# Performance work log

Hardware: AMD Instinct MI355X
Metric: run time of the kernel (lower is better)

The kernel has to match this reference:

```python
import jax, jax.numpy as jnp
import numpy as np

B, S, DMODEL = 1, 2048, 4096
H, HKV, DH = 32, 8, 128
LTAB, RBKT = 20, 128
NEG = -1e9


def rotate_half(x):
    x1, x2 = x[..., : x.shape[-1] // 2], x[..., x.shape[-1] // 2:]
    return jnp.concatenate((-x2, x1), axis=-1)


def setup_inputs() -> dict:
    key = jax.random.key(0)
    ks = jax.random.split(key, 12)
    inp = {
        "hidden_states": jax.random.normal(ks[0], (B, S, DMODEL), jnp.float32),
        "cos": jax.random.uniform(ks[1], (B, S, DH), jnp.float32),
        "sin": jax.random.uniform(ks[2], (B, S, DH), jnp.float32),
        "q_probs": jax.random.uniform(ks[3], (B, H, LTAB, RBKT), jnp.float32),
        "v_norm": jax.random.uniform(ks[4], (B, H, S), jnp.float32),
        "allowed": jnp.ones((B, H, S), dtype=bool),
        "k_hard": jax.random.randint(ks[5], (B, H, LTAB, S), 0, RBKT, jnp.int32),
        "Wq": jax.random.normal(ks[6], (DMODEL, H * DH), jnp.float32) * 0.02,
        "Wk": jax.random.normal(ks[7], (DMODEL, HKV * DH), jnp.float32) * 0.02,
        "Wv": jax.random.normal(ks[8], (DMODEL, HKV * DH), jnp.float32) * 0.02,
        "Wo": jax.random.normal(ks[9], (H * DH, DMODEL), jnp.float32) * 0.02,
        "sink": 4,
        "window": 128,
        "M": 256,
    }
    return inp


def _sparse_key_mask(q_probs, v_norm, allowed, k_hard, sink, window, M):
    """Faithful jax version of build_sparse_list_decode, returned as a boolean
    allowed-key mask [B, H, T] (equivalent to scattering sparse_list)."""
    Bm, Hm, _, T = k_hard.shape
    # soft-hash collision score: sum over tables of q bucket prob at key's bucket,
    # weighted by value-norm history, restricted to allowed keys.
    coll = jnp.take_along_axis(q_probs, k_hard.astype(jnp.int32), axis=-1).sum(axis=2)  # [B,H,T]
    scores = jnp.where(allowed, coll * v_norm, -jnp.inf)
    M_eff = min(M, T)
    mask = jnp.zeros((Bm, Hm, T), dtype=bool)
    if M_eff > 0:
        heavy_idx = jax.lax.top_k(scores, M_eff)[1]  # [B,H,M]
        b_ix = jnp.arange(Bm)[:, None, None]
        h_ix = jnp.arange(Hm)[None, :, None]
        mask = mask.at[b_ix, h_ix, heavy_idx].set(True)
    sink = max(0, min(sink, T))
    window = max(0, min(window, T))
    if sink > 0:
        mask = mask.at[:, :, :sink].set(True)
    if window > 0:
        win_start = max(T - window, sink)
        if win_start < T:
            mask = mask.at[:, :, win_start:].set(True)
    if sink == 0 and window == 0:
        mask = mask.at[:, :, T - 1].set(True)
    return mask & allowed


def reference(hidden_states, cos, sin, q_probs, v_norm, allowed, k_hard,
              Wq, Wk, Wv, Wo, sink, window, M):
    Bx, Sx, _ = hidden_states.shape
    scaling = DH ** -0.5
    q = (hidden_states @ Wq).reshape(Bx, Sx, H, DH).transpose(0, 2, 1, 3)   # [B,H,S,Dh]
    k = (hidden_states @ Wk).reshape(Bx, Sx, HKV, DH).transpose(0, 2, 1, 3)  # [B,Hkv,S,Dh]
    v = (hidden_states @ Wv).reshape(Bx, Sx, HKV, DH).transpose(0, 2, 1, 3)
    # RoPE (unsqueeze_dim=1)
    c, s = cos[:, None, :, :], sin[:, None, :, :]
    q = q * c + rotate_half(q) * s
    k = k * c + rotate_half(k) * s
    # repeat_kv for GQA
    n_rep = H // HKV
    k = jnp.repeat(k, n_rep, axis=1)
    v = jnp.repeat(v, n_rep, axis=1)
    # sparse heavy-hitter + sink + window key mask (no_grad in the original)
    key_mask = _sparse_key_mask(q_probs, v_norm, allowed, k_hard, sink, window, M)  # [B,H,S]
    causal = jnp.tril(jnp.ones((Sx, Sx), dtype=bool))
    allow = causal[None, None] & key_mask[:, :, None, :]  # [B,H,S,S]
    scores = jnp.einsum('bhqd,bhkd->bhqk', q, k) * scaling
    attn = jax.nn.softmax(jnp.where(allow, scores, NEG), axis=-1)
    out = jnp.einsum('bhqk,bhkd->bhqd', attn, v)
    out = out.transpose(0, 2, 1, 3).reshape(Bx, Sx, H * DH)
    return out @ Wo
```

## Files before the change

### kernel.cpp

```cpp
#include <hip/hip_runtime.h>
#include <hip/hip_bf16.h>
#include <cstdint>
#include <cstddef>

namespace {

constexpr int S_LEN = 2048;
constexpr int DM    = 4096;
constexpr int NH    = 32;
constexpr int NKV   = 8;
constexpr int DH    = 128;
constexpr int LTAB  = 20;
constexpr int RBKT  = 128;
constexpr int NQKV  = NH * DH + 2 * NKV * DH;
constexpr int KOFF  = NH * DH;
constexpr int VOFF  = NH * DH + NKV * DH;

typedef short s16x8 __attribute__((ext_vector_type(8)));
typedef float f32x4 __attribute__((ext_vector_type(4)));
typedef unsigned long long u64;
struct u64x2 { u64 x, y; };

__device__ inline short bf16s(float f) {
  __hip_bfloat16 b = __float2bfloat16(f);
  return (short)*reinterpret_cast<unsigned short*>(&b);
}
__device__ inline float s2f(short s) {
  unsigned short u = (unsigned short)s;
  return __bfloat162float(*reinterpret_cast<__hip_bfloat16*>(&u));
}

__device__ inline void transpose64_body(const float* __restrict__ W,
                                        __hip_bfloat16* __restrict__ Wt, int N, int bx,
                                        int by, int tid, float (*tile)[65]) {
  const int kb = by * 64, nb = bx * 64;
  const int r0 = tid >> 4, c4 = (tid & 15) * 4;
#pragma unroll
  for (int it = 0; it < 4; ++it) {
    const int r = r0 + it * 16;
    float4 v = *reinterpret_cast<const float4*>(&W[(size_t)(kb + r) * N + nb + c4]);
    tile[r][c4] = v.x;
    tile[r][c4 + 1] = v.y;
    tile[r][c4 + 2] = v.z;
    tile[r][c4 + 3] = v.w;
  }
  __syncthreads();
  const int n0 = tid >> 4, k4 = (tid & 15) * 4;
#pragma unroll
  for (int it = 0; it < 4; ++it) {
    const int n = n0 + it * 16;
    ushort4 o;
    o.x = (unsigned short)bf16s(tile[k4][n]);
    o.y = (unsigned short)bf16s(tile[k4 + 1][n]);
    o.z = (unsigned short)bf16s(tile[k4 + 2][n]);
    o.w = (unsigned short)bf16s(tile[k4 + 3][n]);
    *reinterpret_cast<ushort4*>(&Wt[(size_t)(nb + n) * DM + kb + k4]) = o;
  }
}

__global__ __launch_bounds__(256) void prep_kernel(
    const float* __restrict__ hidden, const float* __restrict__ Wq,
    const float* __restrict__ Wk, const float* __restrict__ Wv,
    const float* __restrict__ Wo, __hip_bfloat16* __restrict__ hbf,
    __hip_bfloat16* __restrict__ WqkvT, __hip_bfloat16* __restrict__ WoT) {
  __shared__ float tile[64][65];
  const int b = blockIdx.x, tid = threadIdx.x;
  if (b < 2048) {
    const size_t base = (size_t)b * 1024;
#pragma unroll
    for (int it = 0; it < 4; ++it) {
      const size_t i = base + it * 256 + tid;
      float4 v = reinterpret_cast<const float4*>(hidden)[i];
      ushort4 o;
      o.x = (unsigned short)bf16s(v.x);
      o.y = (unsigned short)bf16s(v.y);
      o.z = (unsigned short)bf16s(v.z);
      o.w = (unsigned short)bf16s(v.w);
      reinterpret_cast<ushort4*>(hbf)[i] = o;
    }
    return;
  }
  const float* W;
  __hip_bfloat16* Wt;
  int N, bx, by;
  int t = b - 2048;
  if (t < 4096) {
    W = Wq; Wt = WqkvT; N = DM; bx = t & 63; by = t >> 6;
  } else if (t < 5120) {
    t -= 4096; W = Wk; Wt = WqkvT + (size_t)KOFF * DM; N = NKV * DH; bx = t & 15; by = t >> 4;
  } else if (t < 6144) {
    t -= 5120; W = Wv; Wt = WqkvT + (size_t)VOFF * DM; N = NKV * DH; bx = t & 15; by = t >> 4;
  } else {
    t -= 6144; W = Wo; Wt = WoT; N = DM; bx = t & 63; by = t >> 6;
  }
  transpose64_body(W, Wt, N, bx, by, tid, tile);
}

__global__ __launch_bounds__(1024) void select_kernel(const float* __restrict__ q_probs,
                                                      const float* __restrict__ v_norm,
                                                      const int* __restrict__ allowed,
                                                      const int* __restrict__ k_hard,
                                                      const int* __restrict__ sinkp,
                                                      const int* __restrict__ winp,
                                                      const int* __restrict__ Mp,
                                                      int* __restrict__ sel_idx,
                                                      int* __restrict__ sel_cnt) {
  const int h = blockIdx.x;
  const int tid = threadIdx.x;
  const int lane = tid & 63;
  const int wid = tid >> 6;
  __shared__ u64 keys[S_LEN];
  __shared__ int waveTot[16];
  const int t0 = tid * 2;
  float c0 = 0.f, c1 = 0.f;
#pragma unroll
  for (int l = 0; l < LTAB; ++l) {
    const int2 kh = *reinterpret_cast<const int2*>(&k_hard[(size_t)(h * LTAB + l) * S_LEN + t0]);
    c0 += q_probs[(h * LTAB + l) * RBKT + kh.x];
    c1 += q_probs[(h * LTAB + l) * RBKT + kh.y];
  }
  const int2 al = *reinterpret_cast<const int2*>(&allowed[h * S_LEN + t0]);
  const float2 vn = *reinterpret_cast<const float2*>(&v_norm[h * S_LEN + t0]);
  const float s0 = al.x ? c0 * vn.x : -INFINITY;
  const float s1 = al.y ? c1 * vn.y : -INFINITY;
  auto mkkey = [](float s, int t) -> u64 {
    unsigned m = __float_as_uint(s);
    m = (m & 0x80000000u) ? ~m : (m | 0x80000000u);
    return ((u64)m << 11) | (u64)(S_LEN - 1 - t);
  };
  const u64 k0 = mkkey(s0, t0);
  const u64 k1 = mkkey(s1, t0 + 1);
  keys[t0] = k0;
  keys[t0 + 1] = k1;
  __syncthreads();
  int r0 = 0, r1 = 0;
#pragma unroll 8
  for (int u = 0; u < S_LEN; u += 2) {
    const u64x2 kv = *reinterpret_cast<const u64x2*>(&keys[u]);
    r0 += (kv.x > k0) + (kv.y > k0);
    r1 += (kv.x > k1) + (kv.y > k1);
  }
  const int Mv = min(Mp[0], S_LEN);
  int sv = sinkp[0];
  sv = sv < 0 ? 0 : (sv > S_LEN ? S_LEN : sv);
  int wv = winp[0];
  wv = wv < 0 ? 0 : (wv > S_LEN ? S_LEN : wv);
  int wstart = S_LEN - wv;
  if (wstart < sv) wstart = sv;
  bool sel0 = r0 < Mv, sel1 = r1 < Mv;
  if (t0 < sv) sel0 = true;
  if (t0 + 1 < sv) sel1 = true;
  if (wv > 0) {
    if (t0 >= wstart) sel0 = true;
    if (t0 + 1 >= wstart) sel1 = true;
  }
  if (sv == 0 && wv == 0) {
    if (t0 == S_LEN - 1) sel0 = true;
    if (t0 + 1 == S_LEN - 1) sel1 = true;
  }
  sel0 = sel0 && (al.x != 0);
  sel1 = sel1 && (al.y != 0);
  const int cnt = (sel0 ? 1 : 0) + (sel1 ? 1 : 0);
  int inc = cnt;
#pragma unroll
  for (int off = 1; off < 64; off <<= 1) {
    int n = __shfl_up(inc, off);
    if (lane >= off) inc += n;
  }
  if (lane == 63) waveTot[wid] = inc;
  __syncthreads();
  int wbase = 0;
  for (int w = 0; w < wid; ++w) wbase += waveTot[w];
  int pos = wbase + inc - cnt;
  if (tid == 0) {
    int tot = 0;
#pragma unroll
    for (int w = 0; w < 16; ++w) tot += waveTot[w];
    sel_cnt[h] = tot;
  }
  if (sel0) sel_idx[h * S_LEN + pos++] = t0;
  if (sel1) sel_idx[h * S_LEN + pos] = t0 + 1;
}

template <bool OUT_F32>
__global__ __launch_bounds__(256) void gemm_bt(const __hip_bfloat16* __restrict__ A,
                                               const __hip_bfloat16* __restrict__ Bt,
                                               void* __restrict__ Cout,
                                               int N, int K) {
  __shared__ __hip_bfloat16 As[128 * 64];
  __shared__ __hip_bfloat16 Bs[128 * 64];
  const int tid = threadIdx.x;
  const int wid = tid >> 6;
  const int lane = tid & 63;
  const int bm = blockIdx.y, bn = blockIdx.x;
  const int wr = wid >> 1, wc = wid & 1;
  f32x4 acc[4][4] = {};
  const __hip_bfloat16* Abase = A + (size_t)bm * 128 * K;
  const __hip_bfloat16* Bbase = Bt + (size_t)bn * 128 * K;
  for (int kt = 0; kt < K; kt += 64) {
    __syncthreads();
#pragma unroll
    for (int j = 0; j < 4; ++j) {
      const int pb = j * 4096 + wid * 1024;
      const int p = pb + lane * 16;
      const int row = p >> 7;
      const int slot = ((p >> 4) & 7) ^ (row & 7);
      const int goff = row * K + kt + slot * 8;
      __builtin_amdgcn_global_load_lds(
          (const __attribute__((address_space(1))) void*)(Abase + goff),
          (__attribute__((address_space(3))) void*)(As + (pb >> 1)), 16, 0, 0);
      __builtin_amdgcn_global_load_lds(
          (const __attribute__((address_space(1))) void*)(Bbase + goff),
          (__attribute__((address_space(3))) void*)(Bs + (pb >> 1)), 16, 0, 0);
    }
    __syncthreads();
#pragma unroll
    for (int kk = 0; kk < 2; ++kk) {
      s16x8 af[4], bf[4];
#pragma unroll
      for (int i = 0; i < 4; ++i) {
        const int ra = wr * 64 + i * 16 + (lane & 15);
        const int sa = (kk * 4 + (lane >> 4)) ^ (ra & 7);
        af[i] = *reinterpret_cast<const s16x8*>(As + ra * 64 + sa * 8);
        const int rb = wc * 64 + i * 16 + (lane & 15);
        const int sb = (kk * 4 + (lane >> 4)) ^ (rb & 7);
        bf[i] = *reinterpret_cast<const s16x8*>(Bs + rb * 64 + sb * 8);
      }
#pragma unroll
      for (int i = 0; i < 4; ++i)
#pragma unroll
        for (int jn = 0; jn < 4; ++jn)
          acc[i][jn] = __builtin_amdgcn_mfma_f32_16x16x32_bf16(af[i], bf[jn], acc[i][jn], 0, 0, 0);
    }
  }
  const int rg = (lane >> 4) * 4;
  const int cg = lane & 15;
#pragma unroll
  for (int i = 0; i < 4; ++i)
#pragma unroll
    for (int jn = 0; jn < 4; ++jn)
#pragma unroll
      for (int r = 0; r < 4; ++r) {
        const int rr = bm * 128 + wr * 64 + i * 16 + rg + r;
        const int cc = bn * 128 + wc * 64 + jn * 16 + cg;
        if (OUT_F32)
          reinterpret_cast<float*>(Cout)[(size_t)rr * N + cc] = acc[i][jn][r];
        else
          reinterpret_cast<__hip_bfloat16*>(Cout)[(size_t)rr * N + cc] =
              __float2bfloat16(acc[i][jn][r]);
      }
}

__global__ __launch_bounds__(256) void gemm_bt_splitk(const __hip_bfloat16* __restrict__ A,
                                                      const __hip_bfloat16* __restrict__ Bt,
                                                      float* __restrict__ P,
                                                      int N, int Kfull, int KH) {
  __shared__ __hip_bfloat16 As[128 * 64];
  __shared__ __hip_bfloat16 Bs[128 * 64];
  const int tid = threadIdx.x;
  const int wid = tid >> 6;
  const int lane = tid & 63;
  const int bm = blockIdx.y, bn = blockIdx.x, kz = blockIdx.z;
  const int wr = wid >> 1, wc = wid & 1;
  f32x4 acc[4][4] = {};
  const __hip_bfloat16* Abase = A + (size_t)bm * 128 * Kfull + kz * KH;
  const __hip_bfloat16* Bbase = Bt + (size_t)bn * 128 * Kfull + kz * KH;
  for (int kt = 0; kt < KH; kt += 64) {
    __syncthreads();
#pragma unroll
    for (int j = 0; j < 4; ++j) {
      const int pb = j * 4096 + wid * 1024;
      const int p = pb + lane * 16;
      const int row = p >> 7;
      const int slot = ((p >> 4) & 7) ^ (row & 7);
      const int goff = row * Kfull + kt + slot * 8;
      __builtin_amdgcn_global_load_lds(
          (const __attribute__((address_space(1))) void*)(Abase + goff),
          (__attribute__((address_space(3))) void*)(As + (pb >> 1)), 16, 0, 0);
      __builtin_amdgcn_global_load_lds(
          (const __attribute__((address_space(1))) void*)(Bbase + goff),
          (__attribute__((address_space(3))) void*)(Bs + (pb >> 1)), 16, 0, 0);
    }
    __syncthreads();
#pragma unroll
    for (int kk = 0; kk < 2; ++kk) {
      s16x8 af[4], bf[4];
#pragma unroll
      for (int i = 0; i < 4; ++i) {
        const int ra = wr * 64 + i * 16 + (lane & 15);
        const int sa = (kk * 4 + (lane >> 4)) ^ (ra & 7);
        af[i] = *reinterpret_cast<const s16x8*>(As + ra * 64 + sa * 8);
        const int rb = wc * 64 + i * 16 + (lane & 15);
        const int sb = (kk * 4 + (lane >> 4)) ^ (rb & 7);
        bf[i] = *reinterpret_cast<const s16x8*>(Bs + rb * 64 + sb * 8);
      }
#pragma unroll
      for (int i = 0; i < 4; ++i)
#pragma unroll
        for (int jn = 0; jn < 4; ++jn)
          acc[i][jn] = __builtin_amdgcn_mfma_f32_16x16x32_bf16(af[i], bf[jn], acc[i][jn], 0, 0, 0);
    }
  }
  float* Pz = P + (size_t)kz * S_LEN * N;
  const int rg = (lane >> 4) * 4;
  const int cg = lane & 15;
#pragma unroll
  for (int i = 0; i < 4; ++i)
#pragma unroll
    for (int jn = 0; jn < 4; ++jn)
#pragma unroll
      for (int r = 0; r < 4; ++r) {
        const int rr = bm * 128 + wr * 64 + i * 16 + rg + r;
        const int cc = bn * 128 + wc * 64 + jn * 16 + cg;
        Pz[(size_t)rr * N + cc] = acc[i][jn][r];
      }
}

__global__ __launch_bounds__(256) void reduce_splitk(const float* __restrict__ P,
                                                     float* __restrict__ out, int n4) {
  const int i = blockIdx.x * 256 + threadIdx.x;
  if (i >= n4) return;
  const float4 a = reinterpret_cast<const float4*>(P)[i];
  const float4 b = reinterpret_cast<const float4*>(P + (size_t)S_LEN * DM)[i];
  float4 o;
  o.x = a.x + b.x;
  o.y = a.y + b.y;
  o.z = a.z + b.z;
  o.w = a.w + b.w;
  reinterpret_cast<float4*>(out)[i] = o;
}

__global__ __launch_bounds__(256) void rope_kernel(const __hip_bfloat16* __restrict__ QKV,
                                                   const float* __restrict__ cosb,
                                                   const float* __restrict__ sinb,
                                                   __hip_bfloat16* __restrict__ Qro,
                                                   __hip_bfloat16* __restrict__ Kro) {
  const int s = blockIdx.x;
  const int tid = threadIdx.x;
  const float* cs = cosb + s * DH;
  const float* sn = sinb + s * DH;
  const __hip_bfloat16* row = QKV + (size_t)s * NQKV;
  for (int ch = tid; ch < 512 + 128; ch += 256) {
    const bool isQ = ch < 512;
    const int idx8 = (isQ ? ch : ch - 512) * 8;
    const int d8 = idx8 & (DH - 1);
    const int hb = idx8 - d8;
    const __hip_bfloat16* src = isQ ? row : row + KOFF;
    s16x8 v = *reinterpret_cast<const s16x8*>(src + idx8);
    s16x8 p = *reinterpret_cast<const s16x8*>(src + hb + (d8 ^ 64));
    const float sgn = (d8 < 64) ? -1.f : 1.f;
    s16x8 outv;
#pragma unroll
    for (int j = 0; j < 8; ++j) {
      const float r = s2f(v[j]) * cs[d8 + j] + sgn * s2f(p[j]) * sn[d8 + j];
      outv[j] = bf16s(r);
    }
    if (isQ)
      *reinterpret_cast<s16x8*>(Qro + (size_t)s * (NH * DH) + idx8) = outv;
    else
      *reinterpret_cast<s16x8*>(Kro + (size_t)s * (NKV * DH) + idx8) = outv;
  }
}

__global__ __launch_bounds__(256) void attn_kernel(const __hip_bfloat16* __restrict__ Qro,
                                                   const __hip_bfloat16* __restrict__ Kro,
                                                   const __hip_bfloat16* __restrict__ Vpk,
                                                   const int* __restrict__ sel_idx,
                                                   const int* __restrict__ sel_cnt,
                                                   __hip_bfloat16* __restrict__ ctx) {
  constexpr int BKV = 64;
  const int h = blockIdx.y;
  const int q0 = blockIdx.x * 64;
  const int tid = threadIdx.x, wid = tid >> 6, lane = tid & 63;
  const int l15 = lane & 15, hi = lane >> 4;
  const int kv = h >> 2;
  __shared__ __hip_bfloat16 Ks[BKV][DH + 8];
  __shared__ __hip_bfloat16 Vt[DH][BKV + 8];
  __shared__ __hip_bfloat16 Ps[4][16][BKV + 8];
  __shared__ int tIdx[BKV];
  const int qbase = q0 + wid * 16;
  const float scaling = 0.08838834764831845f;
  s16x8 qf[4];
  {
    const __hip_bfloat16* qp =
        Qro + (size_t)(qbase + l15) * (NH * DH) + h * DH + hi * 8;
#pragma unroll
    for (int kt = 0; kt < 4; ++kt) {
      s16x8 q = *reinterpret_cast<const s16x8*>(qp + kt * 32);
#pragma unroll
      for (int j = 0; j < 8; ++j) q[j] = bf16s(s2f(q[j]) * scaling);
      qf[kt] = q;
    }
  }
  s16x8 ones;
#pragma unroll
  for (int j = 0; j < 8; ++j) ones[j] = (short)0x3F80;
  float mr[4], lr[4];
#pragma unroll
  for (int r = 0; r < 4; ++r) {
    mr[r] = -3.0e38f;
    lr[r] = 0.f;
  }
  f32x4 o[8] = {};
  const int cnt = sel_cnt[h];
  const int qmax = q0 + 63;
  for (int j0 = 0; j0 < cnt; j0 += BKV) {
    if (sel_idx[h * S_LEN + j0] > qmax) break;
    const int nk = min(BKV, cnt - j0);
    __syncthreads();
    if (tid < BKV) tIdx[tid] = (tid < nk) ? sel_idx[h * S_LEN + j0 + tid] : 0x7fffffff;
#pragma unroll
    for (int c = 0; c < 4; ++c) {
      const int ch = tid + c * 256;
      const int row = ch >> 4, c8 = ch & 15;
      if (row < nk) {
        const int t = sel_idx[h * S_LEN + j0 + row];
        *reinterpret_cast<s16x8*>(&Ks[row][c8 * 8]) = *reinterpret_cast<const s16x8*>(
            Kro + (size_t)t * (NKV * DH) + kv * DH + c8 * 8);
      }
    }
    {
      const int j = tid >> 2;
      const int dp = (tid & 3) * 32;
      const int ccA = j ^ (((dp >> 4) & 7) << 3);
      const int ccB = j ^ ((((dp >> 4) + 1) & 7) << 3);
      if (j < nk) {
        const int t = sel_idx[h * S_LEN + j0 + j];
        const __hip_bfloat16* vp = Vpk + (size_t)t * NQKV + kv * DH + dp;
        s16x8 a = *reinterpret_cast<const s16x8*>(vp);
        s16x8 bq = *reinterpret_cast<const s16x8*>(vp + 8);
        s16x8 cq = *reinterpret_cast<const s16x8*>(vp + 16);
        s16x8 dq = *reinterpret_cast<const s16x8*>(vp + 24);
#pragma unroll
        for (int i = 0; i < 8; ++i) reinterpret_cast<short&>(Vt[dp + i][ccA]) = a[i];
#pragma unroll
        for (int i = 0; i < 8; ++i) reinterpret_cast<short&>(Vt[dp + 8 + i][ccA]) = bq[i];
#pragma unroll
        for (int i = 0; i < 8; ++i) reinterpret_cast<short&>(Vt[dp + 16 + i][ccB]) = cq[i];
#pragma unroll
        for (int i = 0; i < 8; ++i) reinterpret_cast<short&>(Vt[dp + 24 + i][ccB]) = dq[i];
      } else {
#pragma unroll
        for (int i = 0; i < 16; ++i) reinterpret_cast<short&>(Vt[dp + i][ccA]) = 0;
#pragma unroll
        for (int i = 0; i < 16; ++i) reinterpret_cast<short&>(Vt[dp + 16 + i][ccB]) = 0;
      }
    }
    __syncthreads();
    f32x4 sc[4];
#pragma unroll
    for (int kc = 0; kc < 4; ++kc) sc[kc] = f32x4{0.f, 0.f, 0.f, 0.f};
#pragma unroll
    for (int kt = 0; kt < 4; ++kt) {
#pragma unroll
      for (int kc = 0; kc < 4; ++kc) {
        const s16x8 kf =
            *reinterpret_cast<const s16x8*>(&Ks[kc * 16 + l15][kt * 32 + hi * 8]);
        sc[kc] = __builtin_amdgcn_mfma_f32_16x16x32_bf16(qf[kt], kf, sc[kc], 0, 0, 0);
      }
    }
    int tt[4];
#pragma unroll
    for (int kc = 0; kc < 4; ++kc) tt[kc] = tIdx[kc * 16 + l15];
    float vv[4][4];
    bool need = false;
#pragma unroll
    for (int r = 0; r < 4; ++r) {
      const int qs = qbase + (hi << 2) + r;
      float mx = -3.0e38f;
#pragma unroll
      for (int kc = 0; kc < 4; ++kc) {
        vv[kc][r] = (tt[kc] <= qs) ? sc[kc][r] : -1.0e9f;
        mx = fmaxf(mx, vv[kc][r]);
      }
      need = need || (mx > mr[r] + 8.f);
    }
    if (__any(need)) {
#pragma unroll
      for (int r = 0; r < 4; ++r) {
        float m = fmaxf(fmaxf(vv[0][r], vv[1][r]), fmaxf(vv[2][r], vv[3][r]));
#pragma unroll
        for (int off = 1; off < 16; off <<= 1) m = fmaxf(m, __shfl_xor(m, off));
        const float mn = fmaxf(mr[r], m);
        const float scl = __expf(mr[r] - mn);
        lr[r] *= scl;
#pragma unroll
        for (int nt = 0; nt < 8; ++nt) o[nt][r] *= scl;
        mr[r] = mn;
      }
    }
#pragma unroll
    for (int r = 0; r < 4; ++r) {
#pragma unroll
      for (int kc = 0; kc < 4; ++kc) {
        Ps[wid][(hi << 2) + r][kc * 16 + l15] = __float2bfloat16(__expf(vv[kc][r] - mr[r]));
      }
    }
    const s16x8 pf0 = *reinterpret_cast<const s16x8*>(&Ps[wid][l15][hi * 8]);
    const s16x8 pf1 = *reinterpret_cast<const s16x8*>(&Ps[wid][l15][32 + hi * 8]);
    {
      f32x4 zero = {0.f, 0.f, 0.f, 0.f};
      f32x4 ps = __builtin_amdgcn_mfma_f32_16x16x32_bf16(pf0, ones, zero, 0, 0, 0);
      ps = __builtin_amdgcn_mfma_f32_16x16x32_bf16(pf1, ones, ps, 0, 0, 0);
#pragma unroll
      for (int r = 0; r < 4; ++r) lr[r] += ps[r];
    }
#pragma unroll
    for (int nt = 0; nt < 8; ++nt) {
      const s16x8 vfa =
          *reinterpret_cast<const s16x8*>(&Vt[nt * 16 + l15][(hi * 8) ^ (nt * 8)]);
      const s16x8 vfb =
          *reinterpret_cast<const s16x8*>(&Vt[nt * 16 + l15][(32 + hi * 8) ^ (nt * 8)]);
      o[nt] = __builtin_amdgcn_mfma_f32_16x16x32_bf16(pf0, vfa, o[nt], 0, 0, 0);
      o[nt] = __builtin_amdgcn_mfma_f32_16x16x32_bf16(pf1, vfb, o[nt], 0, 0, 0);
    }
  }
#pragma unroll
  for (int nt = 0; nt < 8; ++nt)
#pragma unroll
    for (int r = 0; r < 4; ++r) {
      const int qs = qbase + (hi << 2) + r;
      const int d = nt * 16 + l15;
      ctx[(size_t)qs * (NH * DH) + h * DH + d] = __float2bfloat16(o[nt][r] / lr[r]);
    }
}

}

extern "C" void kernel_launch(void* const* d_in, const int* in_sizes, int n_in,
                              void* d_out, int out_size, void* d_ws, size_t ws_size,
                              hipStream_t stream) {
  const float* hidden = (const float*)d_in[0];
  const float* cosb = (const float*)d_in[1];
  const float* sinb = (const float*)d_in[2];
  const float* q_probs = (const float*)d_in[3];
  const float* v_norm = (const float*)d_in[4];
  const int* allowed = (const int*)d_in[5];
  const int* k_hard = (const int*)d_in[6];
  const float* Wq = (const float*)d_in[7];
  const float* Wk = (const float*)d_in[8];
  const float* Wv = (const float*)d_in[9];
  const float* Wo = (const float*)d_in[10];
  const int* sinkp = (const int*)d_in[11];
  const int* winp = (const int*)d_in[12];
  const int* Mp = (const int*)d_in[13];

  char* ws = (char*)d_ws;
  size_t off = 0;
  auto alloc = [&](size_t bytes) -> char* {
    char* p = ws + off;
    off += (bytes + 255) & ~(size_t)255;
    return p;
  };
  __hip_bfloat16* hbf = (__hip_bfloat16*)alloc((size_t)S_LEN * DM * 2);
  __hip_bfloat16* WqkvT = (__hip_bfloat16*)alloc((size_t)NQKV * DM * 2);
  __hip_bfloat16* WoT = (__hip_bfloat16*)alloc((size_t)DM * DM * 2);
  __hip_bfloat16* QKV = (__hip_bfloat16*)alloc((size_t)S_LEN * NQKV * 2);
  __hip_bfloat16* Qro = (__hip_bfloat16*)alloc((size_t)S_LEN * NH * DH * 2);
  __hip_bfloat16* Kro = (__hip_bfloat16*)alloc((size_t)S_LEN * NKV * DH * 2);
  __hip_bfloat16* ctx = (__hip_bfloat16*)alloc((size_t)S_LEN * NH * DH * 2);
  int* sel_idx = (int*)alloc((size_t)NH * S_LEN * 4);
  int* sel_cnt = (int*)alloc((size_t)NH * 4);
  if (off > ws_size) return;
  float* Psplit = (float*)hbf;

  prep_kernel<<<12288, 256, 0, stream>>>(hidden, Wq, Wk, Wv, Wo, hbf, WqkvT, WoT);

  select_kernel<<<NH, 1024, 0, stream>>>(q_probs, v_norm, allowed, k_hard, sinkp, winp, Mp,
                                         sel_idx, sel_cnt);

  gemm_bt<false><<<dim3(NQKV / 128, S_LEN / 128), 256, 0, stream>>>(
      hbf, WqkvT, (void*)QKV, NQKV, DM);

  rope_kernel<<<S_LEN, 256, 0, stream>>>(QKV, cosb, sinb, Qro, Kro);

  attn_kernel<<<dim3(S_LEN / 64, NH), 256, 0, stream>>>(Qro, Kro, QKV + VOFF, sel_idx,
                                                        sel_cnt, ctx);

  gemm_bt_splitk<<<dim3(DM / 128, S_LEN / 128, 2), 256, 0, stream>>>(ctx, WoT, Psplit, DM,
                                                                     DM, DM / 2);
  reduce_splitk<<<(S_LEN * DM / 4 + 255) / 256, 256, 0, stream>>>((const float*)Psplit,
                                                                  (float*)d_out,
                                                                  S_LEN * DM / 4);
}
```

Before: 409.4 us.

## Fuse RoPE into QKV GEMM epilogue and prefetch attention K/V tiles into registers

The QKV projection GEMM now stages its output tile through shared memory and applies RoPE to Q and K columns in the epilogue, writing rotated values in place. This removes the separate rope kernel launch and its extra global read and write of Q and K. The attention kernel reads Q, K and V directly from the packed QKV buffer. It also double-buffers K/V gathers in registers, loading the next tile while the current one is computed, to hide gather latency. In exchange the GEMM epilogue gains two barriers and per-row cos/sin loads, and the attention kernel uses more registers.

```diff
diff --git a/kernel.cpp b/kernel.cpp
--- a/kernel.cpp
+++ b/kernel.cpp
@@ -182,13 +182,15 @@
   if (sel1) sel_idx[h * S_LEN + pos] = t0 + 1;
 }
 
-template <bool OUT_F32>
-__global__ __launch_bounds__(256) void gemm_bt(const __hip_bfloat16* __restrict__ A,
-                                               const __hip_bfloat16* __restrict__ Bt,
-                                               void* __restrict__ Cout,
-                                               int N, int K) {
-  __shared__ __hip_bfloat16 As[128 * 64];
-  __shared__ __hip_bfloat16 Bs[128 * 64];
+__global__ __launch_bounds__(256) void gemm_qkv_rope(const __hip_bfloat16* __restrict__ A,
+                                                     const __hip_bfloat16* __restrict__ Bt,
+                                                     __hip_bfloat16* __restrict__ Cout,
+                                                     const float* __restrict__ cosb,
+                                                     const float* __restrict__ sinb) {
+  __shared__ __hip_bfloat16 smbuf[128 * 136];
+  __hip_bfloat16* As = smbuf;
+  __hip_bfloat16* Bs = smbuf + 128 * 64;
+  constexpr int N = NQKV, K = DM;
   const int tid = threadIdx.x;
   const int wid = tid >> 6;
   const int lane = tid & 63;
@@ -233,6 +235,7 @@
           acc[i][jn] = __builtin_amdgcn_mfma_f32_16x16x32_bf16(af[i], bf[jn], acc[i][jn], 0, 0, 0);
     }
   }
+  __syncthreads();
   const int rg = (lane >> 4) * 4;
   const int cg = lane & 15;
 #pragma unroll
@@ -240,15 +243,32 @@
 #pragma unroll
     for (int jn = 0; jn < 4; ++jn)
 #pragma unroll
-      for (int r = 0; r < 4; ++r) {
-        const int rr = bm * 128 + wr * 64 + i * 16 + rg + r;
-        const int cc = bn * 128 + wc * 64 + jn * 16 + cg;
-        if (OUT_F32)
-          reinterpret_cast<float*>(Cout)[(size_t)rr * N + cc] = acc[i][jn][r];
-        else
-          reinterpret_cast<__hip_bfloat16*>(Cout)[(size_t)rr * N + cc] =
-              __float2bfloat16(acc[i][jn][r]);
-      }
+      for (int r = 0; r < 4; ++r)
+        smbuf[(wr * 64 + i * 16 + rg + r) * 136 + wc * 64 + jn * 16 + cg] =
+            __float2bfloat16(acc[i][jn][r]);
+  __syncthreads();
+  const bool isV = (bn * 128) >= VOFF;
+  const int srow = tid >> 1;
+  const int col0 = (tid & 1) * 64;
+  const int sg = bm * 128 + srow;
+#pragma unroll
+  for (int c = 0; c < 8; ++c) {
+    const int d0 = col0 + ((c + srow) & 7) * 8;
+    s16x8 x = *reinterpret_cast<const s16x8*>(&smbuf[srow * 136 + d0]);
+    s16x8 outv;
+    if (isV) {
+      outv = x;
+    } else {
+      const s16x8 xp = *reinterpret_cast<const s16x8*>(&smbuf[srow * 136 + (d0 ^ 64)]);
+      const float sgn = (d0 < 64) ? -1.f : 1.f;
+      const float* cs = cosb + (size_t)sg * DH + d0;
+      const float* sn = sinb + (size_t)sg * DH + d0;
+#pragma unroll
+      for (int j = 0; j < 8; ++j)
+        outv[j] = bf16s(s2f(x[j]) * cs[j] + sgn * s2f(xp[j]) * sn[j]);
+    }
+    *reinterpret_cast<s16x8*>(&Cout[(size_t)sg * N + bn * 128 + d0]) = outv;
+  }
 }
 
 __global__ __launch_bounds__(256) void gemm_bt_splitk(const __hip_bfloat16* __restrict__ A,
@@ -330,41 +350,7 @@
   reinterpret_cast<float4*>(out)[i] = o;
 }
 
-__global__ __launch_bounds__(256) void rope_kernel(const __hip_bfloat16* __restrict__ QKV,
-                                                   const float* __restrict__ cosb,
-                                                   const float* __restrict__ sinb,
-                                                   __hip_bfloat16* __restrict__ Qro,
-                                                   __hip_bfloat16* __restrict__ Kro) {
-  const int s = blockIdx.x;
-  const int tid = threadIdx.x;
-  const float* cs = cosb + s * DH;
-  const float* sn = sinb + s * DH;
-  const __hip_bfloat16* row = QKV + (size_t)s * NQKV;
-  for (int ch = tid; ch < 512 + 128; ch += 256) {
-    const bool isQ = ch < 512;
-    const int idx8 = (isQ ? ch : ch - 512) * 8;
-    const int d8 = idx8 & (DH - 1);
-    const int hb = idx8 - d8;
-    const __hip_bfloat16* src = isQ ? row : row + KOFF;
-    s16x8 v = *reinterpret_cast<const s16x8*>(src + idx8);
-    s16x8 p = *reinterpret_cast<const s16x8*>(src + hb + (d8 ^ 64));
-    const float sgn = (d8 < 64) ? -1.f : 1.f;
-    s16x8 outv;
-#pragma unroll
-    for (int j = 0; j < 8; ++j) {
-      const float r = s2f(v[j]) * cs[d8 + j] + sgn * s2f(p[j]) * sn[d8 + j];
-      outv[j] = bf16s(r);
-    }
-    if (isQ)
-      *reinterpret_cast<s16x8*>(Qro + (size_t)s * (NH * DH) + idx8) = outv;
-    else
-      *reinterpret_cast<s16x8*>(Kro + (size_t)s * (NKV * DH) + idx8) = outv;
-  }
-}
-
-__global__ __launch_bounds__(256) void attn_kernel(const __hip_bfloat16* __restrict__ Qro,
-                                                   const __hip_bfloat16* __restrict__ Kro,
-                                                   const __hip_bfloat16* __restrict__ Vpk,
+__global__ __launch_bounds__(256) void attn_kernel(const __hip_bfloat16* __restrict__ Qkv,
                                                    const int* __restrict__ sel_idx,
                                                    const int* __restrict__ sel_cnt,
                                                    __hip_bfloat16* __restrict__ ctx) {
@@ -383,7 +369,7 @@
   s16x8 qf[4];
   {
     const __hip_bfloat16* qp =
-        Qro + (size_t)(qbase + l15) * (NH * DH) + h * DH + hi * 8;
+        Qkv + (size_t)(qbase + l15) * NQKV + h * DH + hi * 8;
 #pragma unroll
     for (int kt = 0; kt < 4; ++kt) {
       s16x8 q = *reinterpret_cast<const s16x8*>(qp + kt * 32);
@@ -404,115 +390,129 @@
   f32x4 o[8] = {};
   const int cnt = sel_cnt[h];
   const int qmax = q0 + 63;
-  for (int j0 = 0; j0 < cnt; j0 += BKV) {
-    if (sel_idx[h * S_LEN + j0] > qmax) break;
+
+  int tIdxReg = 0x7fffffff;
+  s16x8 rK[4];
+  s16x8 rV[4];
+  const int vj = tid >> 2, vdp = (tid & 3) * 32;
+
+  auto load_tile = [&](int j0) {
     const int nk = min(BKV, cnt - j0);
-    __syncthreads();
-    if (tid < BKV) tIdx[tid] = (tid < nk) ? sel_idx[h * S_LEN + j0 + tid] : 0x7fffffff;
+    if (tid < BKV) tIdxReg = (tid < nk) ? sel_idx[h * S_LEN + j0 + tid] : 0x7fffffff;
 #pragma unroll
     for (int c = 0; c < 4; ++c) {
       const int ch = tid + c * 256;
       const int row = ch >> 4, c8 = ch & 15;
-      if (row < nk) {
-        const int t = sel_idx[h * S_LEN + j0 + row];
-        *reinterpret_cast<s16x8*>(&Ks[row][c8 * 8]) = *reinterpret_cast<const s16x8*>(
-            Kro + (size_t)t * (NKV * DH) + kv * DH + c8 * 8);
-      }
-    }
-    {
-      const int j = tid >> 2;
-      const int dp = (tid & 3) * 32;
-      const int ccA = j ^ (((dp >> 4) & 7) << 3);
-      const int ccB = j ^ ((((dp >> 4) + 1) & 7) << 3);
-      if (j < nk) {
-        const int t = sel_idx[h * S_LEN + j0 + j];
-        const __hip_bfloat16* vp = Vpk + (size_t)t * NQKV + kv * DH + dp;
-        s16x8 a = *reinterpret_cast<const s16x8*>(vp);
-        s16x8 bq = *reinterpret_cast<const s16x8*>(vp + 8);
-        s16x8 cq = *reinterpret_cast<const s16x8*>(vp + 16);
-        s16x8 dq = *reinterpret_cast<const s16x8*>(vp + 24);
-#pragma unroll
-        for (int i = 0; i < 8; ++i) reinterpret_cast<short&>(Vt[dp + i][ccA]) = a[i];
-#pragma unroll
-        for (int i = 0; i < 8; ++i) reinterpret_cast<short&>(Vt[dp + 8 + i][ccA]) = bq[i];
-#pragma unroll
-        for (int i = 0; i < 8; ++i) reinterpret_cast<short&>(Vt[dp + 16 + i][ccB]) = cq[i];
-#pragma unroll
-        for (int i = 0; i < 8; ++i) reinterpret_cast<short&>(Vt[dp + 24 + i][ccB]) = dq[i];
-      } else {
-#pragma unroll
-        for (int i = 0; i < 16; ++i) reinterpret_cast<short&>(Vt[dp + i][ccA]) = 0;
-#pragma unroll
-        for (int i = 0; i < 16; ++i) reinterpret_cast<short&>(Vt[dp + 16 + i][ccB]) = 0;
-      }
-    }
-    __syncthreads();
-    f32x4 sc[4];
-#pragma unroll
-    for (int kc = 0; kc < 4; ++kc) sc[kc] = f32x4{0.f, 0.f, 0.f, 0.f};
-#pragma unroll
-    for (int kt = 0; kt < 4; ++kt) {
-#pragma unroll
-      for (int kc = 0; kc < 4; ++kc) {
-        const s16x8 kf =
-            *reinterpret_cast<const s16x8*>(&Ks[kc * 16 + l15][kt * 32 + hi * 8]);
-        sc[kc] = __builtin_amdgcn_mfma_f32_16x16x32_bf16(qf[kt], kf, sc[kc], 0, 0, 0);
-      }
-    }
-    int tt[4];
-#pragma unroll
-    for (int kc = 0; kc < 4; ++kc) tt[kc] = tIdx[kc * 16 + l15];
-    float vv[4][4];
-    bool need = false;
-#pragma unroll
-    for (int r = 0; r < 4; ++r) {
-      const int qs = qbase + (hi << 2) + r;
-      float mx = -3.0e38f;
-#pragma unroll
-      for (int kc = 0; kc < 4; ++kc) {
-        vv[kc][r] = (tt[kc] <= qs) ? sc[kc][r] : -1.0e9f;
-        mx = fmaxf(mx, vv[kc][r]);
-      }
-      need = need || (mx > mr[r] + 8.f);
-    }
-    if (__any(need)) {
+      const int t = sel_idx[h * S_LEN + j0 + min(row, nk - 1)];
+      rK[c] = *reinterpret_cast<const s16x8*>(Qkv + (size_t)t * NQKV + KOFF + kv * DH + c8 * 8);
+    }
+    if (vj < nk) {
+      const int t = sel_idx[h * S_LEN + j0 + vj];
+      const __hip_bfloat16* vp = Qkv + (size_t)t * NQKV + VOFF + kv * DH + vdp;
+#pragma unroll
+      for (int c = 0; c < 4; ++c) rV[c] = *reinterpret_cast<const s16x8*>(vp + c * 8);
+    } else {
+#pragma unroll
+      for (int c = 0; c < 4; ++c) rV[c] = s16x8{};
+    }
+  };
+
+  if (cnt > 0 && sel_idx[h * S_LEN] <= qmax) {
+    load_tile(0);
+    for (int j0 = 0; j0 < cnt; j0 += BKV) {
+      const int nk = min(BKV, cnt - j0);
+      __syncthreads();
+      if (tid < BKV) tIdx[tid] = tIdxReg;
+#pragma unroll
+      for (int c = 0; c < 4; ++c) {
+        const int ch = tid + c * 256;
+        const int row = ch >> 4, c8 = ch & 15;
+        if (row < nk) *reinterpret_cast<s16x8*>(&Ks[row][c8 * 8]) = rK[c];
+      }
+      {
+        const int ccA = vj ^ (((vdp >> 4) & 7) << 3);
+        const int ccB = vj ^ ((((vdp >> 4) + 1) & 7) << 3);
+#pragma unroll
+        for (int i = 0; i < 8; ++i) reinterpret_cast<short&>(Vt[vdp + i][ccA]) = rV[0][i];
+#pragma unroll
+        for (int i = 0; i < 8; ++i) reinterpret_cast<short&>(Vt[vdp + 8 + i][ccA]) = rV[1][i];
+#pragma unroll
+        for (int i = 0; i < 8; ++i) reinterpret_cast<short&>(Vt[vdp + 16 + i][ccB]) = rV[2][i];
+#pragma unroll
+        for (int i = 0; i < 8; ++i) reinterpret_cast<short&>(Vt[vdp + 24 + i][ccB]) = rV[3][i];
+      }
+      const int jn0 = j0 + BKV;
+      const bool more = (jn0 < cnt) && (sel_idx[h * S_LEN + jn0] <= qmax);
+      if (more) load_tile(jn0);
+      __syncthreads();
+      f32x4 sc[4];
+#pragma unroll
+      for (int kc = 0; kc < 4; ++kc) sc[kc] = f32x4{0.f, 0.f, 0.f, 0.f};
+#pragma unroll
+      for (int kt = 0; kt < 4; ++kt) {
+#pragma unroll
+        for (int kc = 0; kc < 4; ++kc) {
+          const s16x8 kf =
+              *reinterpret_cast<const s16x8*>(&Ks[kc * 16 + l15][kt * 32 + hi * 8]);
+          sc[kc] = __builtin_amdgcn_mfma_f32_16x16x32_bf16(qf[kt], kf, sc[kc], 0, 0, 0);
+        }
+      }
+      int tt[4];
+#pragma unroll
+      for (int kc = 0; kc < 4; ++kc) tt[kc] = tIdx[kc * 16 + l15];
+      float vv[4][4];
+      bool need = false;
 #pragma unroll
       for (int r = 0; r < 4; ++r) {
-        float m = fmaxf(fmaxf(vv[0][r], vv[1][r]), fmaxf(vv[2][r], vv[3][r]));
-#pragma unroll
-        for (int off = 1; off < 16; off <<= 1) m = fmaxf(m, __shfl_xor(m, off));
-        const float mn = fmaxf(mr[r], m);
-        const float scl = __expf(mr[r] - mn);
-        lr[r] *= scl;
-#pragma unroll
-        for (int nt = 0; nt < 8; ++nt) o[nt][r] *= scl;
-        mr[r] = mn;
-      }
-    }
-#pragma unroll
-    for (int r = 0; r < 4; ++r) {
-#pragma unroll
-      for (int kc = 0; kc < 4; ++kc) {
-        Ps[wid][(hi << 2) + r][kc * 16 + l15] = __float2bfloat16(__expf(vv[kc][r] - mr[r]));
-      }
-    }
-    const s16x8 pf0 = *reinterpret_cast<const s16x8*>(&Ps[wid][l15][hi * 8]);
-    const s16x8 pf1 = *reinterpret_cast<const s16x8*>(&Ps[wid][l15][32 + hi * 8]);
-    {
-      f32x4 zero = {0.f, 0.f, 0.f, 0.f};
-      f32x4 ps = __builtin_amdgcn_mfma_f32_16x16x32_bf16(pf0, ones, zero, 0, 0, 0);
-      ps = __builtin_amdgcn_mfma_f32_16x16x32_bf16(pf1, ones, ps, 0, 0, 0);
-#pragma unroll
-      for (int r = 0; r < 4; ++r) lr[r] += ps[r];
-    }
-#pragma unroll
-    for (int nt = 0; nt < 8; ++nt) {
-      const s16x8 vfa =
-          *reinterpret_cast<const s16x8*>(&Vt[nt * 16 + l15][(hi * 8) ^ (nt * 8)]);
-      const s16x8 vfb =
-          *reinterpret_cast<const s16x8*>(&Vt[nt * 16 + l15][(32 + hi * 8) ^ (nt * 8)]);
-      o[nt] = __builtin_amdgcn_mfma_f32_16x16x32_bf16(pf0, vfa, o[nt], 0, 0, 0);
-      o[nt] = __builtin_amdgcn_mfma_f32_16x16x32_bf16(pf1, vfb, o[nt], 0, 0, 0);
+        const int qs = qbase + (hi << 2) + r;
+        float mx = -3.0e38f;
+#pragma unroll
+        for (int kc = 0; kc < 4; ++kc) {
+          vv[kc][r] = (tt[kc] <= qs) ? sc[kc][r] : -1.0e9f;
+          mx = fmaxf(mx, vv[kc][r]);
+        }
+        need = need || (mx > mr[r] + 8.f);
+      }
+      if (__any(need)) {
+#pragma unroll
+        for (int r = 0; r < 4; ++r) {
+          float m = fmaxf(fmaxf(vv[0][r], vv[1][r]), fmaxf(vv[2][r], vv[3][r]));
+#pragma unroll
+          for (int off = 1; off < 16; off <<= 1) m = fmaxf(m, __shfl_xor(m, off));
+          const float mn = fmaxf(mr[r], m);
+          const float scl = __expf(mr[r] - mn);
+          lr[r] *= scl;
+#pragma unroll
+          for (int nt = 0; nt < 8; ++nt) o[nt][r] *= scl;
+          mr[r] = mn;
+        }
+      }
+#pragma unroll
+      for (int r = 0; r < 4; ++r) {
+#pragma unroll
+        for (int kc = 0; kc < 4; ++kc) {
+          Ps[wid][(hi << 2) + r][kc * 16 + l15] = __float2bfloat16(__expf(vv[kc][r] - mr[r]));
+        }
+      }
+      const s16x8 pf0 = *reinterpret_cast<const s16x8*>(&Ps[wid][l15][hi * 8]);
+      const s16x8 pf1 = *reinterpret_cast<const s16x8*>(&Ps[wid][l15][32 + hi * 8]);
+      {
+        f32x4 zero = {0.f, 0.f, 0.f, 0.f};
+        f32x4 ps = __builtin_amdgcn_mfma_f32_16x16x32_bf16(pf0, ones, zero, 0, 0, 0);
+        ps = __builtin_amdgcn_mfma_f32_16x16x32_bf16(pf1, ones, ps, 0, 0, 0);
+#pragma unroll
+        for (int r = 0; r < 4; ++r) lr[r] += ps[r];
+      }
+#pragma unroll
+      for (int nt = 0; nt < 8; ++nt) {
+        const s16x8 vfa =
+            *reinterpret_cast<const s16x8*>(&Vt[nt * 16 + l15][(hi * 8) ^ (nt * 8)]);
+        const s16x8 vfb =
+            *reinterpret_cast<const s16x8*>(&Vt[nt * 16 + l15][(32 + hi * 8) ^ (nt * 8)]);
+        o[nt] = __builtin_amdgcn_mfma_f32_16x16x32_bf16(pf0, vfa, o[nt], 0, 0, 0);
+        o[nt] = __builtin_amdgcn_mfma_f32_16x16x32_bf16(pf1, vfb, o[nt], 0, 0, 0);
+      }
+      if (!more) break;
     }
   }
 #pragma unroll
@@ -556,8 +556,6 @@
   __hip_bfloat16* WqkvT = (__hip_bfloat16*)alloc((size_t)NQKV * DM * 2);
   __hip_bfloat16* WoT = (__hip_bfloat16*)alloc((size_t)DM * DM * 2);
   __hip_bfloat16* QKV = (__hip_bfloat16*)alloc((size_t)S_LEN * NQKV * 2);
-  __hip_bfloat16* Qro = (__hip_bfloat16*)alloc((size_t)S_LEN * NH * DH * 2);
-  __hip_bfloat16* Kro = (__hip_bfloat16*)alloc((size_t)S_LEN * NKV * DH * 2);
   __hip_bfloat16* ctx = (__hip_bfloat16*)alloc((size_t)S_LEN * NH * DH * 2);
   int* sel_idx = (int*)alloc((size_t)NH * S_LEN * 4);
   int* sel_cnt = (int*)alloc((size_t)NH * 4);
@@ -569,13 +567,10 @@
   select_kernel<<<NH, 1024, 0, stream>>>(q_probs, v_norm, allowed, k_hard, sinkp, winp, Mp,
                                          sel_idx, sel_cnt);
 
-  gemm_bt<false><<<dim3(NQKV / 128, S_LEN / 128), 256, 0, stream>>>(
-      hbf, WqkvT, (void*)QKV, NQKV, DM);
-
-  rope_kernel<<<S_LEN, 256, 0, stream>>>(QKV, cosb, sinb, Qro, Kro);
-
-  attn_kernel<<<dim3(S_LEN / 64, NH), 256, 0, stream>>>(Qro, Kro, QKV + VOFF, sel_idx,
-                                                        sel_cnt, ctx);
+  gemm_qkv_rope<<<dim3(NQKV / 128, S_LEN / 128), 256, 0, stream>>>(hbf, WqkvT, QKV, cosb,
+                                                                   sinb);
+
+  attn_kernel<<<dim3(S_LEN / 64, NH), 256, 0, stream>>>(QKV, sel_idx, sel_cnt, ctx);
 
   gemm_bt_splitk<<<dim3(DM / 128, S_LEN / 128, 2), 256, 0, stream>>>(ctx, WoT, Psplit, DM,
                                                                      DM, DM / 2);
```

Result: slower. 435.4 us (+6.4%).

## Register-prefetch next sparse K/V tile during attention compute

Applied to the files above, without the earlier changes.

The sparse attention loop now loads the next tile's gathered K and V rows, plus the selected indices, into registers before computing on the current tile. After the barrier, those registers are stored to shared memory. This lets the global gather latency overlap with the MFMA and softmax work instead of stalling every iteration. The cost is extra register pressure from the eight s16x8 buffers, which may lower occupancy.

```diff
diff --git a/kernel.cpp b/kernel.cpp
--- a/kernel.cpp
+++ b/kernel.cpp
@@ -404,115 +404,129 @@
   f32x4 o[8] = {};
   const int cnt = sel_cnt[h];
   const int qmax = q0 + 63;
-  for (int j0 = 0; j0 < cnt; j0 += BKV) {
-    if (sel_idx[h * S_LEN + j0] > qmax) break;
+
+  int tIdxReg = 0x7fffffff;
+  s16x8 rK[4];
+  s16x8 rV[4];
+  const int vj = tid >> 2, vdp = (tid & 3) * 32;
+
+  auto load_tile = [&](int j0) {
     const int nk = min(BKV, cnt - j0);
-    __syncthreads();
-    if (tid < BKV) tIdx[tid] = (tid < nk) ? sel_idx[h * S_LEN + j0 + tid] : 0x7fffffff;
+    if (tid < BKV) tIdxReg = (tid < nk) ? sel_idx[h * S_LEN + j0 + tid] : 0x7fffffff;
 #pragma unroll
     for (int c = 0; c < 4; ++c) {
       const int ch = tid + c * 256;
       const int row = ch >> 4, c8 = ch & 15;
-      if (row < nk) {
-        const int t = sel_idx[h * S_LEN + j0 + row];
-        *reinterpret_cast<s16x8*>(&Ks[row][c8 * 8]) = *reinterpret_cast<const s16x8*>(
-            Kro + (size_t)t * (NKV * DH) + kv * DH + c8 * 8);
-      }
-    }
-    {
-      const int j = tid >> 2;
-      const int dp = (tid & 3) * 32;
-      const int ccA = j ^ (((dp >> 4) & 7) << 3);
-      const int ccB = j ^ ((((dp >> 4) + 1) & 7) << 3);
-      if (j < nk) {
-        const int t = sel_idx[h * S_LEN + j0 + j];
-        const __hip_bfloat16* vp = Vpk + (size_t)t * NQKV + kv * DH + dp;
-        s16x8 a = *reinterpret_cast<const s16x8*>(vp);
-        s16x8 bq = *reinterpret_cast<const s16x8*>(vp + 8);
-        s16x8 cq = *reinterpret_cast<const s16x8*>(vp + 16);
-        s16x8 dq = *reinterpret_cast<const s16x8*>(vp + 24);
-#pragma unroll
-        for (int i = 0; i < 8; ++i) reinterpret_cast<short&>(Vt[dp + i][ccA]) = a[i];
-#pragma unroll
-        for (int i = 0; i < 8; ++i) reinterpret_cast<short&>(Vt[dp + 8 + i][ccA]) = bq[i];
-#pragma unroll
-        for (int i = 0; i < 8; ++i) reinterpret_cast<short&>(Vt[dp + 16 + i][ccB]) = cq[i];
-#pragma unroll
-        for (int i = 0; i < 8; ++i) reinterpret_cast<short&>(Vt[dp + 24 + i][ccB]) = dq[i];
-      } else {
-#pragma unroll
-        for (int i = 0; i < 16; ++i) reinterpret_cast<short&>(Vt[dp + i][ccA]) = 0;
-#pragma unroll
-        for (int i = 0; i < 16; ++i) reinterpret_cast<short&>(Vt[dp + 16 + i][ccB]) = 0;
-      }
-    }
-    __syncthreads();
-    f32x4 sc[4];
-#pragma unroll
-    for (int kc = 0; kc < 4; ++kc) sc[kc] = f32x4{0.f, 0.f, 0.f, 0.f};
-#pragma unroll
-    for (int kt = 0; kt < 4; ++kt) {
-#pragma unroll
-      for (int kc = 0; kc < 4; ++kc) {
-        const s16x8 kf =
-            *reinterpret_cast<const s16x8*>(&Ks[kc * 16 + l15][kt * 32 + hi * 8]);
-        sc[kc] = __builtin_amdgcn_mfma_f32_16x16x32_bf16(qf[kt], kf, sc[kc], 0, 0, 0);
-      }
-    }
-    int tt[4];
-#pragma unroll
-    for (int kc = 0; kc < 4; ++kc) tt[kc] = tIdx[kc * 16 + l15];
-    float vv[4][4];
-    bool need = false;
-#pragma unroll
-    for (int r = 0; r < 4; ++r) {
-      const int qs = qbase + (hi << 2) + r;
-      float mx = -3.0e38f;
-#pragma unroll
-      for (int kc = 0; kc < 4; ++kc) {
-        vv[kc][r] = (tt[kc] <= qs) ? sc[kc][r] : -1.0e9f;
-        mx = fmaxf(mx, vv[kc][r]);
-      }
-      need = need || (mx > mr[r] + 8.f);
-    }
-    if (__any(need)) {
+      const int t = sel_idx[h * S_LEN + j0 + min(row, nk - 1)];
+      rK[c] = *reinterpret_cast<const s16x8*>(Kro + (size_t)t * (NKV * DH) + kv * DH + c8 * 8);
+    }
+    if (vj < nk) {
+      const int t = sel_idx[h * S_LEN + j0 + vj];
+      const __hip_bfloat16* vp = Vpk + (size_t)t * NQKV + kv * DH + vdp;
+#pragma unroll
+      for (int c = 0; c < 4; ++c) rV[c] = *reinterpret_cast<const s16x8*>(vp + c * 8);
+    } else {
+#pragma unroll
+      for (int c = 0; c < 4; ++c) rV[c] = s16x8{};
+    }
+  };
+
+  if (cnt > 0 && sel_idx[h * S_LEN] <= qmax) {
+    load_tile(0);
+    for (int j0 = 0; j0 < cnt; j0 += BKV) {
+      const int nk = min(BKV, cnt - j0);
+      __syncthreads();
+      if (tid < BKV) tIdx[tid] = tIdxReg;
+#pragma unroll
+      for (int c = 0; c < 4; ++c) {
+        const int ch = tid + c * 256;
+        const int row = ch >> 4, c8 = ch & 15;
+        if (row < nk) *reinterpret_cast<s16x8*>(&Ks[row][c8 * 8]) = rK[c];
+      }
+      {
+        const int ccA = vj ^ (((vdp >> 4) & 7) << 3);
+        const int ccB = vj ^ ((((vdp >> 4) + 1) & 7) << 3);
+#pragma unroll
+        for (int i = 0; i < 8; ++i) reinterpret_cast<short&>(Vt[vdp + i][ccA]) = rV[0][i];
+#pragma unroll
+        for (int i = 0; i < 8; ++i) reinterpret_cast<short&>(Vt[vdp + 8 + i][ccA]) = rV[1][i];
+#pragma unroll
+        for (int i = 0; i < 8; ++i) reinterpret_cast<short&>(Vt[vdp + 16 + i][ccB]) = rV[2][i];
+#pragma unroll
+        for (int i = 0; i < 8; ++i) reinterpret_cast<short&>(Vt[vdp + 24 + i][ccB]) = rV[3][i];
+      }
+      const int jn0 = j0 + BKV;
+      const bool more = (jn0 < cnt) && (sel_idx[h * S_LEN + jn0] <= qmax);
+      if (more) load_tile(jn0);
+      __syncthreads();
+      f32x4 sc[4];
+#pragma unroll
+      for (int kc = 0; kc < 4; ++kc) sc[kc] = f32x4{0.f, 0.f, 0.f, 0.f};
+#pragma unroll
+      for (int kt = 0; kt < 4; ++kt) {
+#pragma unroll
+        for (int kc = 0; kc < 4; ++kc) {
+          const s16x8 kf =
+              *reinterpret_cast<const s16x8*>(&Ks[kc * 16 + l15][kt * 32 + hi * 8]);
+          sc[kc] = __builtin_amdgcn_mfma_f32_16x16x32_bf16(qf[kt], kf, sc[kc], 0, 0, 0);
+        }
+      }
+      int tt[4];
+#pragma unroll
+      for (int kc = 0; kc < 4; ++kc) tt[kc] = tIdx[kc * 16 + l15];
+      float vv[4][4];
+      bool need = false;
 #pragma unroll
       for (int r = 0; r < 4; ++r) {
-        float m = fmaxf(fmaxf(vv[0][r], vv[1][r]), fmaxf(vv[2][r], vv[3][r]));
-#pragma unroll
-        for (int off = 1; off < 16; off <<= 1) m = fmaxf(m, __shfl_xor(m, off));
-        const float mn = fmaxf(mr[r], m);
-        const float scl = __expf(mr[r] - mn);
-        lr[r] *= scl;
-#pragma unroll
-        for (int nt = 0; nt < 8; ++nt) o[nt][r] *= scl;
-        mr[r] = mn;
-      }
-    }
-#pragma unroll
-    for (int r = 0; r < 4; ++r) {
-#pragma unroll
-      for (int kc = 0; kc < 4; ++kc) {
-        Ps[wid][(hi << 2) + r][kc * 16 + l15] = __float2bfloat16(__expf(vv[kc][r] - mr[r]));
-      }
-    }
-    const s16x8 pf0 = *reinterpret_cast<const s16x8*>(&Ps[wid][l15][hi * 8]);
-    const s16x8 pf1 = *reinterpret_cast<const s16x8*>(&Ps[wid][l15][32 + hi * 8]);
-    {
-      f32x4 zero = {0.f, 0.f, 0.f, 0.f};
-      f32x4 ps = __builtin_amdgcn_mfma_f32_16x16x32_bf16(pf0, ones, zero, 0, 0, 0);
-      ps = __builtin_amdgcn_mfma_f32_16x16x32_bf16(pf1, ones, ps, 0, 0, 0);
-#pragma unroll
-      for (int r = 0; r < 4; ++r) lr[r] += ps[r];
-    }
-#pragma unroll
-    for (int nt = 0; nt < 8; ++nt) {
-      const s16x8 vfa =
-          *reinterpret_cast<const s16x8*>(&Vt[nt * 16 + l15][(hi * 8) ^ (nt * 8)]);
-      const s16x8 vfb =
-          *reinterpret_cast<const s16x8*>(&Vt[nt * 16 + l15][(32 + hi * 8) ^ (nt * 8)]);
-      o[nt] = __builtin_amdgcn_mfma_f32_16x16x32_bf16(pf0, vfa, o[nt], 0, 0, 0);
-      o[nt] = __builtin_amdgcn_mfma_f32_16x16x32_bf16(pf1, vfb, o[nt], 0, 0, 0);
+        const int qs = qbase + (hi << 2) + r;
+        float mx = -3.0e38f;
+#pragma unroll
+        for (int kc = 0; kc < 4; ++kc) {
+          vv[kc][r] = (tt[kc] <= qs) ? sc[kc][r] : -1.0e9f;
+          mx = fmaxf(mx, vv[kc][r]);
+        }
+        need = need || (mx > mr[r] + 8.f);
+      }
+      if (__any(need)) {
+#pragma unroll
+        for (int r = 0; r < 4; ++r) {
+          float m = fmaxf(fmaxf(vv[0][r], vv[1][r]), fmaxf(vv[2][r], vv[3][r]));
+#pragma unroll
+          for (int off = 1; off < 16; off <<= 1) m = fmaxf(m, __shfl_xor(m, off));
+          const float mn = fmaxf(mr[r], m);
+          const float scl = __expf(mr[r] - mn);
+          lr[r] *= scl;
+#pragma unroll
+          for (int nt = 0; nt < 8; ++nt) o[nt][r] *= scl;
+          mr[r] = mn;
+        }
+      }
+#pragma unroll
+      for (int r = 0; r < 4; ++r) {
+#pragma unroll
+        for (int kc = 0; kc < 4; ++kc) {
+          Ps[wid][(hi << 2) + r][kc * 16 + l15] = __float2bfloat16(__expf(vv[kc][r] - mr[r]));
+        }
+      }
+      const s16x8 pf0 = *reinterpret_cast<const s16x8*>(&Ps[wid][l15][hi * 8]);
+      const s16x8 pf1 = *reinterpret_cast<const s16x8*>(&Ps[wid][l15][32 + hi * 8]);
+      {
+        f32x4 zero = {0.f, 0.f, 0.f, 0.f};
+        f32x4 ps = __builtin_amdgcn_mfma_f32_16x16x32_bf16(pf0, ones, zero, 0, 0, 0);
+        ps = __builtin_amdgcn_mfma_f32_16x16x32_bf16(pf1, ones, ps, 0, 0, 0);
+#pragma unroll
+        for (int r = 0; r < 4; ++r) lr[r] += ps[r];
+      }
+#pragma unroll
+      for (int nt = 0; nt < 8; ++nt) {
+        const s16x8 vfa =
+            *reinterpret_cast<const s16x8*>(&Vt[nt * 16 + l15][(hi * 8) ^ (nt * 8)]);
+        const s16x8 vfb =
+            *reinterpret_cast<const s16x8*>(&Vt[nt * 16 + l15][(32 + hi * 8) ^ (nt * 8)]);
+        o[nt] = __builtin_amdgcn_mfma_f32_16x16x32_bf16(pf0, vfa, o[nt], 0, 0, 0);
+        o[nt] = __builtin_amdgcn_mfma_f32_16x16x32_bf16(pf1, vfb, o[nt], 0, 0, 0);
+      }
+      if (!more) break;
     }
   }
 #pragma unroll
```

Result: faster. 395.3 us (-3.4%).
